# Optimization experiments

Hardware: AMD Instinct MI355X
Metric: run time of the kernel (lower is better)

The kernel has to match this reference:

```python
import jax, jax.numpy as jnp
import numpy as np
import math

N_NODES = 16384
N_EDGES = 200000
RADIUS = 2.5
BOX = 42.5
NUM_NEIGHBORS = 3.8

# irreps as (mul, l, parity); parity=-1 => irreps_sh = 1x0e+1x1o+1x2e+1x3o
IRREPS_SH = [(1,0,1),(1,1,-1),(1,2,1),(1,3,-1)]
GATE_IN = [(16,0,1),(16,0,-1),(8,0,1),(8,0,-1),(8,0,1),(8,0,-1),(16,1,-1),(16,1,1)]
GATE_OUT = [(16,0,1),(16,0,-1),(16,1,-1),(16,1,1)]
FINAL_OUT = [(1,1,-1)]

def _cg_coef(j1,m1,j2,m2,j3,m3):
    f = math.factorial
    pref = math.sqrt((2*j3+1)*f(j3+j1-j2)*f(j3-j1+j2)*f(j1+j2-j3)/f(j1+j2+j3+1))
    pref *= math.sqrt(f(j3+m3)*f(j3-m3)*f(j1-m1)*f(j1+m1)*f(j2-m2)*f(j2+m2))
    s = 0.0
    for k in range(j1+j2-j3+1):
        args = (k, j1+j2-j3-k, j1-m1-k, j2+m2-k, j3-j2+m1+k, j3-j1-m2+k)
        if min(args) < 0:
            continue
        d = 1
        for a in args:
            d *= f(a)
        s += (-1)**k / d
    return pref*s

def _cg_complex(l1,l2,l3):
    C = np.zeros((2*l1+1,2*l2+1,2*l3+1))
    for m1 in range(-l1,l1+1):
        for m2 in range(-l2,l2+1):
            m3 = m1+m2
            if abs(m3) <= l3:
                C[m1+l1,m2+l2,m3+l3] = _cg_coef(l1,m1,l2,m2,l3,m3)
    return C

def _u(l):
    # complex -> real spherical-harmonics change of basis (m ordered -l..l)
    U = np.zeros((2*l+1,2*l+1), dtype=complex)
    U[l,l] = 1.0
    for m in range(1,l+1):
        U[l+m,l+m] = (-1)**m/math.sqrt(2); U[l+m,l-m] = 1/math.sqrt(2)
        U[l-m,l-m] = 1j/math.sqrt(2);      U[l-m,l+m] = -1j*(-1)**m/math.sqrt(2)
    return U

_CG = {}
def cg_real(l1,l2,l3):
    k = (l1,l2,l3)
    if k not in _CG:
        C = np.einsum('au,bv,cw,uvw->abc', _u(l1), _u(l2), _u(l3).conj(), _cg_complex(l1,l2,l3).astype(complex))
        Cr = C.imag if np.abs(C.imag).sum() > np.abs(C.real).sum() else C.real
        _CG[k] = jnp.asarray(Cr.astype(np.float32))
    return _CG[k]

def _slices(irr):
    out, off = [], 0
    for (m,l,p) in irr:
        out.append((off,m,l,p)); off += m*(2*l+1)
    return out

def weight_numel(irr1, irr2, irro):
    n = 0
    for (_,m1,l1,p1) in _slices(irr1):
        for (_,m2,l2,p2) in _slices(irr2):
            for (_,mo,lo,po) in _slices(irro):
                if po == p1*p2 and abs(l1-l2) <= lo <= l1+l2:
                    n += m1*m2*mo
    return n

def fctp(x1, x2, w, irr1, irr2, irro):
    # fully-connected tensor product with per-edge external weights
    s1, s2, so = _slices(irr1), _slices(irr2), _slices(irro)
    E = x1.shape[0]
    chunks = [jnp.zeros((E,m,2*l+1), dtype=x1.dtype) for (_,m,l,_) in so]
    fan = [0]*len(so)
    woff = 0
    for (o1,m1,l1,p1) in s1:
        for (o2,m2,l2,p2) in s2:
            for io,(oo,mo,lo,po) in enumerate(so):
                if po == p1*p2 and abs(l1-l2) <= lo <= l1+l2:
                    nw = m1*m2*mo
                    wp = w[:, woff:woff+nw].reshape(E,m1,m2,mo); woff += nw
                    a = x1[:, o1:o1+m1*(2*l1+1)].reshape(E,m1,2*l1+1)
                    b = x2[:, o2:o2+m2*(2*l2+1)].reshape(E,m2,2*l2+1)
                    chunks[io] = chunks[io] + jnp.einsum('euvw,eui,evj,ijk->ewk', wp, a, b, cg_real(l1,l2,lo))
                    fan[io] += m1*m2
    return jnp.concatenate([(c/math.sqrt(f) if f > 0 else c).reshape(E,-1) for c,f in zip(chunks,fan)], axis=1)

def sph_harm(u):
    # real SH l=0..3, component normalization, m=-l..l, on unit vectors
    x, y, z = u[:,0], u[:,1], u[:,2]
    s3, s5, s15 = math.sqrt(3.), math.sqrt(5.), math.sqrt(15.)
    c33, c32, c31, c30, c3p2 = math.sqrt(35/8), math.sqrt(105.), math.sqrt(21/8), 0.5*math.sqrt(7.), 0.5*math.sqrt(105.)
    comps = [jnp.ones_like(x),
             s3*y, s3*z, s3*x,
             s15*x*y, s15*y*z, 0.5*s5*(3*z*z-1.), s15*x*z, 0.5*s15*(x*x-y*y),
             c33*y*(3*x*x-y*y), c32*x*y*z, c31*y*(5*z*z-1.), c30*(5*z**3-3*z),
             c31*x*(5*z*z-1.), c3p2*z*(x*x-y*y), c33*x*(x*x-3*y*y)]
    return jnp.stack(comps, axis=1)

def soft_one_hot(r):
    # basis='smooth_finite', cutoff=True, start=0.5, end=2.5, number=3
    centers = jnp.array([1.0, 1.5, 2.0], dtype=r.dtype)
    d = (r[:,None] - centers) / 0.5
    d2 = d*d
    inside = d2 < 1.0
    safe = jnp.where(inside, d2, 0.0)
    return jnp.where(inside, 1.14136*(math.e**2)*jnp.exp(1.0/(safe-1.0)), 0.0)

def gate_fn(x):
    se = jax.nn.relu(x[:,0:16]); so = jnp.abs(x[:,16:32])
    g = jnp.concatenate([jax.nn.relu(x[:,32:40]), jnp.tanh(x[:,40:48]),
                         jax.nn.relu(x[:,48:56]), jnp.tanh(x[:,56:64])], axis=1)  # [N,32]
    v1o = x[:,64:112].reshape(-1,16,3) * g[:,0:16,None]
    v1e = x[:,112:160].reshape(-1,16,3) * g[:,16:32,None]
    return jnp.concatenate([se, so, v1o.reshape(-1,48), v1e.reshape(-1,48)], axis=1)

def _forward(position, edge_src, edge_dst, W1, W2, W1f, W2f):
    evec = position[edge_src] - position[edge_dst]           # [E,3]
    r = jnp.linalg.norm(evec, axis=1)
    ea = sph_harm(evec / r[:,None])                          # [E,16]
    es = soft_one_hot(r) * math.sqrt(3.0)                    # [E,3]
    inv = 1.0/math.sqrt(NUM_NEIGHBORS)
    x = jax.ops.segment_sum(ea, edge_dst, num_segments=N_NODES) * inv      # [N,16]
    w = (jax.nn.relu(es @ W1 / math.sqrt(3.0)) @ W2) / math.sqrt(256.0)    # [E,272]
    e = fctp(x[edge_src], ea, w, IRREPS_SH, IRREPS_SH, GATE_IN)            # [E,160]
    x = jax.ops.segment_sum(e, edge_dst, num_segments=N_NODES) * inv       # [N,160]
    x = gate_fn(x)                                                          # [N,128]
    wf = (jax.nn.relu(es @ W1f / math.sqrt(3.0)) @ W2f) / math.sqrt(256.0) # [E,64]
    e = fctp(x[edge_src], ea, wf, GATE_OUT, IRREPS_SH, FINAL_OUT)          # [E,3]
    return jax.ops.segment_sum(e, edge_dst, num_segments=N_NODES) * inv    # [N,3]

def setup_inputs():
    rng = np.random.RandomState(0)
    pos = (rng.rand(N_NODES,3) * BOX).astype(np.float32)
    n2 = (pos**2).sum(1)
    src_l, dst_l = [], []
    for i0 in range(0, N_NODES, 2048):
        p = pos[i0:i0+2048]
        d2 = n2[i0:i0+2048,None] + n2[None,:] - 2.0*(p @ pos.T)
        ii, jj = np.nonzero(d2 < RADIUS*RADIUS)
        ii = ii + i0
        m = ii != jj
        src_l.append(jj[m]); dst_l.append(ii[m])
    src = np.concatenate(src_l); dst = np.concatenate(dst_l)
    if len(src) < N_EDGES:
        reps = int(np.ceil(N_EDGES/max(len(src),1)))
        src = np.tile(src, reps); dst = np.tile(dst, reps)
    src = src[:N_EDGES].astype(np.int32); dst = dst[:N_EDGES].astype(np.int32)
    key = jax.random.key(0)
    k1, k2, k3, k4 = jax.random.split(key, 4)
    w2n = weight_numel(IRREPS_SH, IRREPS_SH, GATE_IN)    # 272
    w2fn = weight_numel(GATE_OUT, IRREPS_SH, FINAL_OUT)  # 64
    return {"position": jnp.asarray(pos), "edge_src": jnp.asarray(src), "edge_dst": jnp.asarray(dst),
            "W1": jax.random.normal(k1,(3,256),jnp.float32), "W2": jax.random.normal(k2,(256,w2n),jnp.float32),
            "W1f": jax.random.normal(k3,(3,256),jnp.float32), "W2f": jax.random.normal(k4,(256,w2fn),jnp.float32)}

def reference(position, edge_src, edge_dst, W1, W2, W1f, W2f):
    return _forward(position, edge_src, edge_dst, W1, W2, W1f, W2f)
```

## Files before the change

### kernel.cpp

```cpp
#include <hip/hip_runtime.h>
#include <cmath>

#define T_TAB 3072
#define NN 16384
#define NG 4
#define CH2 16

struct CD { double re, im; };
constexpr CD cmul(CD a, CD b){ return {a.re*b.re - a.im*b.im, a.re*b.im + a.im*b.re}; }
constexpr CD cadd(CD a, CD b){ return {a.re+b.re, a.im+b.im}; }
constexpr CD conj_(CD a){ return {a.re, -a.im}; }
constexpr CD cscale(CD a, double s){ return {a.re*s, a.im*s}; }
constexpr double cfabs_(double x){ return x<0.0 ? -x : x; }
constexpr double csqrt_(double x){
  double g = x > 1.0 ? x : 1.0;
  for (int i=0;i<80;++i) g = 0.5*(g + x/g);
  return g;
}
constexpr double factd(int n){ double r=1.0; for(int i=2;i<=n;++i) r*=(double)i; return r; }

constexpr double cg_coef(int j1,int m1,int j2,int m2,int j3,int m3){
  double pref = csqrt_((2.0*j3+1.0)*factd(j3+j1-j2)*factd(j3-j1+j2)*factd(j1+j2-j3)/factd(j1+j2+j3+1));
  pref *= csqrt_(factd(j3+m3)*factd(j3-m3)*factd(j1-m1)*factd(j1+m1)*factd(j2-m2)*factd(j2+m2));
  double s=0.0;
  for(int k=0;k<=j1+j2-j3;++k){
    int a0=k,a1=j1+j2-j3-k,a2=j1-m1-k,a3=j2+m2-k,a4=j3-j2+m1+k,a5=j3-j1-m2+k;
    if(a0<0||a1<0||a2<0||a3<0||a4<0||a5<0) continue;
    double d=factd(a0)*factd(a1)*factd(a2)*factd(a3)*factd(a4)*factd(a5);
    s += ((k&1)?-1.0:1.0)/d;
  }
  return pref*s;
}

struct UMat { CD u[7][7]; };
constexpr UMat u_fill(int l){
  UMat M{};
  const double is2 = csqrt_(0.5);
  M.u[l][l] = CD{1.0, 0.0};
  for(int m=1;m<=l;++m){
    double sgn = (m&1)?-1.0:1.0;
    M.u[l+m][l+m] = CD{sgn*is2, 0.0};
    M.u[l+m][l-m] = CD{is2, 0.0};
    M.u[l-m][l-m] = CD{0.0, is2};
    M.u[l-m][l+m] = CD{0.0, -sgn*is2};
  }
  return M;
}

template<int L1,int L2,int L3>
struct FT { float v[(2*L1+1)*(2*L2+1)*(2*L3+1)]; };

template<int L1,int L2,int L3>
constexpr FT<L1,L2,L3> cg_real_ct(){
  constexpr int n1=2*L1+1, n2=2*L2+1, n3=2*L3+1;
  double Cc[7][7][7] = {};
  for(int m1=-L1;m1<=L1;++m1)
    for(int m2=-L2;m2<=L2;++m2){
      int m3=m1+m2;
      if(m3>=-L3&&m3<=L3) Cc[m1+L1][m2+L2][m3+L3]=cg_coef(L1,m1,L2,m2,L3,m3);
    }
  UMat U1 = u_fill(L1), U2 = u_fill(L2), U3 = u_fill(L3);
  CD Cr[7][7][7] = {};
  double sre=0.0, sim=0.0;
  for(int a=0;a<n1;++a)for(int b=0;b<n2;++b)for(int c=0;c<n3;++c){
    CD acc{0.0,0.0};
    for(int u=0;u<n1;++u)for(int v=0;v<n2;++v){
      int w = (u-L1)+(v-L2)+L3;
      if (w < 0 || w >= n3) continue;
      double cc = Cc[u][v][w];
      if (cc == 0.0) continue;
      acc = cadd(acc, cscale(cmul(cmul(U1.u[a][u],U2.u[b][v]),conj_(U3.u[c][w])), cc));
    }
    Cr[a][b][c] = acc;
    sre += cfabs_(acc.re); sim += cfabs_(acc.im);
  }
  FT<L1,L2,L3> out{};
  bool useim = sim > sre;
  for(int a=0;a<n1;++a)for(int b=0;b<n2;++b)for(int c=0;c<n3;++c)
    out.v[(a*n2+b)*n3+c] = (float)(useim ? Cr[a][b][c].im : Cr[a][b][c].re);
  return out;
}

constexpr auto CG000 = cg_real_ct<0,0,0>();
constexpr auto CG110 = cg_real_ct<1,1,0>();
constexpr auto CG220 = cg_real_ct<2,2,0>();
constexpr auto CG330 = cg_real_ct<3,3,0>();
constexpr auto CG011 = cg_real_ct<0,1,1>();
constexpr auto CG101 = cg_real_ct<1,0,1>();
constexpr auto CG111 = cg_real_ct<1,1,1>();
constexpr auto CG121 = cg_real_ct<1,2,1>();
constexpr auto CG211 = cg_real_ct<2,1,1>();
constexpr auto CG221 = cg_real_ct<2,2,1>();
constexpr auto CG231 = cg_real_ct<2,3,1>();
constexpr auto CG321 = cg_real_ct<3,2,1>();
constexpr auto CG331 = cg_real_ct<3,3,1>();

#define TERM(TBL, IDX, PROD, ACC) { float c_ = TBL.v[IDX]; if (c_ != 0.0f) ACC = fmaf((PROD), c_, ACC); }

__device__ __forceinline__ void afadd(float* p, float v){ unsafeAtomicAdd(p, v); }

__device__ __forceinline__ float soh(float r, float c){
  float d = (r - c) * 2.0f;
  float d2 = d*d;
  return (d2 < 1.0f) ? 1.14136f * expf(2.0f + 1.0f/(d2-1.0f)) : 0.0f;
}

__device__ __forceinline__ float bf_lo(unsigned u){ return __uint_as_float(u << 16); }
__device__ __forceinline__ float bf_hi(unsigned u){ return __uint_as_float(u & 0xFFFF0000u); }
__device__ __forceinline__ unsigned short bfpack(float v){
  unsigned b = __float_as_uint(v);
  return (unsigned short)((b + 0x7FFFu + ((b >> 16) & 1u)) >> 16);
}
__device__ __forceinline__ void unp8(uint4 u, float* o){
  o[0]=bf_lo(u.x); o[1]=bf_hi(u.x); o[2]=bf_lo(u.y); o[3]=bf_hi(u.y);
  o[4]=bf_lo(u.z); o[5]=bf_hi(u.z); o[6]=bf_lo(u.w); o[7]=bf_hi(u.w);
}

__device__ __forceinline__ void lane_sched(int lane, int q, int& col, int& slot){
  col = -1; slot = 31;
  if (lane < 16){
    int s = q >> 2, qq = q & 3;
    int a = 2*lane + s;
    const int base0[4] = {0, 64, 144, 224};
    col = base0[qq] + a; slot = qq;
  } else if (lane < 40){
    int idx = lane-16, u = idx/3, k = idx-3*u;
    const int wb[6] = {32,48,112,128,192,208};
    const int sb[6] = {4,7,10,13,16,19};
    if (q < 6){ col = wb[q]+u; slot = sb[q]+k; }
  } else if (lane < 52){
    int m = lane-40;
    int c0 = (q < 4) ? 2*m : 2*m+1;
    int u = c0/3, k = c0-3*u;
    int qq = (q < 4) ? q : q-4;
    if (qq < 3){
      const int wb[3] = {96,176,256};
      const int sb[3] = {22,25,28};
      col = wb[qq]+u; slot = sb[qq]+k;
    }
  }
}

#define TBLK 1008
#define RPB  65
__global__ __launch_bounds__(256) void k_stageA(
    const float* __restrict__ W1, const float* __restrict__ W2,
    const float* __restrict__ W1f, const float* __restrict__ W2f,
    float* __restrict__ tab1, unsigned short* __restrict__ tab2b,
    const int* __restrict__ dst, int E, int* __restrict__ rowptr,
    float* __restrict__ out, int outN)
{
  const int bid = blockIdx.x;
  if (bid < TBLK){
    const int jq  = bid / 12;
    const int t   = (bid % 12)*256 + threadIdx.x;
    const int j0  = jq*4;
    const float dr = 2.5f / (float)(T_TAB-1);
    const float r = (float)t * dr;
    const float e0 = soh(r,1.0f), e1 = soh(r,1.5f), e2 = soh(r,2.0f);
    float ax=0.f, ay=0.f, az=0.f, aw=0.f;
    if (j0 < 272){
      for (int cc=0; cc<256; ++cc){
        float h = fmaxf(fmaf(e0,W1[cc], fmaf(e1,W1[256+cc], e2*W1[512+cc])), 0.0f);
        float4 w = *(const float4*)(W2 + cc*272 + j0);
        ax = fmaf(h,w.x,ax); ay = fmaf(h,w.y,ay);
        az = fmaf(h,w.z,az); aw = fmaf(h,w.w,aw);
      }
      *(float4*)(tab1 + (size_t)t*272 + j0) = make_float4(ax*0.0625f, ay*0.0625f, az*0.0625f, aw*0.0625f);
    } else {
      const int jj = j0 - 272;
      for (int cc=0; cc<256; ++cc){
        float h = fmaxf(fmaf(e0,W1f[cc], fmaf(e1,W1f[256+cc], e2*W1f[512+cc])), 0.0f);
        float4 w = *(const float4*)(W2f + cc*64 + jj);
        ax = fmaf(h,w.x,ax); ay = fmaf(h,w.y,ay);
        az = fmaf(h,w.z,az); aw = fmaf(h,w.w,aw);
      }
      ushort4 o;
      o.x = bfpack(ax*0.0625f); o.y = bfpack(ay*0.0625f);
      o.z = bfpack(az*0.0625f); o.w = bfpack(aw*0.0625f);
      *(ushort4*)(tab2b + (size_t)t*64 + jj) = o;
    }
  } else if (bid < TBLK + RPB){
    const int n = (bid-TBLK)*256 + threadIdx.x;
    if (n > NN) return;
    int lo=0, hi=E;
    while (lo < hi){ int mid=(lo+hi)>>1; if (dst[mid] < n) lo=mid+1; else hi=mid; }
    rowptr[n]=lo;
  } else {
    const int idx = (bid - TBLK - RPB)*256 + threadIdx.x;
    if (idx < outN) out[idx] = 0.0f;
  }
}

#define PERB 6144
__global__ __launch_bounds__(256) void k_stageB(
    const float* __restrict__ tab1, unsigned short* __restrict__ tabP,
    const float* __restrict__ pos, const int* __restrict__ src,
    const int* __restrict__ rowptr, float* __restrict__ xacc)
{
  const int bid = blockIdx.x;
  if (bid < PERB){
    const int gid = bid*256 + threadIdx.x;
    const int t = gid >> 9, p = gid & 511;
    int col, slot;
    lane_sched(p>>3, p&7, col, slot);
    float v = (col >= 0) ? tab1[(size_t)t*272 + col] : 0.0f;
    tabP[gid] = bfpack(v);
    return;
  }
  const int tt = (bid-PERB)*256 + threadIdx.x;
  const int n = tt>>2, q = tt&3;
  if (n>=NN) return;
  const int r0=rowptr[n], r1=rowptr[n+1];
  const float pdx=pos[3*n], pdy=pos[3*n+1], pdz=pos[3*n+2];
  const float s3=1.73205081f, s5=2.23606798f, s15=3.87298335f;
  const float c33=2.09165007f, c32=10.2469508f, c31=1.62018517f, c30=1.32287566f, cp2=5.12347538f;
  float a0=0,a1=0,a2=0,a3=0,a4=0,a5=0,a6=0,a7=0,a8=0,a9=0,a10=0,a11=0,a12=0,a13=0,a14=0,a15=0;
  for (int e=r0+q; e<r1; e+=4){
    const int s=src[e];
    float ax=pos[3*s]-pdx, ay=pos[3*s+1]-pdy, az=pos[3*s+2]-pdz;
    float ir = 1.0f/sqrtf(ax*ax+ay*ay+az*az);
    float x=ax*ir, y=ay*ir, z=az*ir;
    a0+=1.0f; a1+=s3*y; a2+=s3*z; a3+=s3*x;
    a4+=s15*x*y; a5+=s15*y*z; a6+=0.5f*s5*(3.0f*z*z-1.0f); a7+=s15*x*z;
    a8+=0.5f*s15*(x*x-y*y); a9+=c33*y*(3.0f*x*x-y*y); a10+=c32*x*y*z; a11+=c31*y*(5.0f*z*z-1.0f);
    a12+=c30*(5.0f*z*z*z-3.0f*z); a13+=c31*x*(5.0f*z*z-1.0f); a14+=cp2*z*(x*x-y*y);
    a15+=c33*x*(x*x-3.0f*y*y);
  }
#define RED(v) v += __shfl_xor(v,1); v += __shfl_xor(v,2);
  RED(a0) RED(a1) RED(a2) RED(a3) RED(a4) RED(a5) RED(a6) RED(a7)
  RED(a8) RED(a9) RED(a10) RED(a11) RED(a12) RED(a13) RED(a14) RED(a15)
#undef RED
  float o0,o1,o2,o3;
  if (q==0){ o0=a0; o1=a1; o2=a2; o3=a3; }
  else if (q==1){ o0=a4; o1=a5; o2=a6; o3=a7; }
  else if (q==2){ o0=a8; o1=a9; o2=a10; o3=a11; }
  else { o0=a12; o1=a13; o2=a14; o3=a15; }
  *(float4*)(xacc + (size_t)n*16 + q*4) = make_float4(o0,o1,o2,o3);
}

__global__ __launch_bounds__(64) void k_tp1(
    const float* __restrict__ pos, const int* __restrict__ src,
    const int* __restrict__ rowptr, const float* __restrict__ xacc,
    const unsigned short* __restrict__ tabP, unsigned short* __restrict__ xgb)
{
  const int lane = threadIdx.x;
  const int nb   = blockIdx.x*NG;
  const int g    = lane >> 4, je = lane & 15;
  __shared__ float SI[NG][CH2][33];
  __shared__ int   SiT[NG][CH2];
  __shared__ float SG[NG][32];

  int rp[NG+1];
#pragma unroll
  for (int q=0;q<=NG;++q) rp[q] = rowptr[nb+q];
  int deg[NG];
#pragma unroll
  for (int q=0;q<NG;++q) deg[q] = rp[q+1]-rp[q];
  const int dmax = max(max(deg[0],deg[1]), max(deg[2],deg[3]));
  const int nch = (dmax + CH2 - 1) / CH2;

  int ioS[8];
#pragma unroll
  for (int p=0;p<8;++p){ int c_, s_; lane_sched(lane, p, c_, s_); ioS[p] = s_; }
  int gu0=16, gu1=16;
  if (lane >= 16 && lane < 40){ gu0 = 16 + (lane-16)/3; }
  else if (lane >= 40 && lane < 52){
    int m=lane-40; gu0 = 24 + (2*m)/3; gu1 = 24 + (2*m+1)/3;
  }

  const int mynode = nb + g;
  const float pdx=pos[3*mynode], pdy=pos[3*mynode+1], pdz=pos[3*mynode+2];
  float acc0[NG]={0,0,0,0}, acc1[NG]={0,0,0,0};

  for (int t=0; t<nch; ++t){
    __syncthreads();
    const int cg_ = deg[g] - t*CH2;
    if (je < cg_){
      const int e = rp[g] + t*CH2 + je;
      const int s = src[e];
      float ax=pos[3*s]-pdx, ay=pos[3*s+1]-pdy, az=pos[3*s+2]-pdz;
      float r = sqrtf(ax*ax+ay*ay+az*az);
      float ir = 1.0f/r;
      float x=ax*ir, y=ay*ir, z=az*ir;
      float f = r * 1228.4f;
      int i0 = (int)(f + 0.5f);
      if (i0 > T_TAB-1) i0 = T_TAB-1;

      const float s3=1.73205081f, s5=2.23606798f, s15=3.87298335f;
      const float c33=2.09165007f, c32=10.2469508f, c31=1.62018517f, c30=1.32287566f, cp2=5.12347538f;
      float Y[16];
      Y[0]=1.0f;
      Y[1]=s3*y; Y[2]=s3*z; Y[3]=s3*x;
      Y[4]=s15*x*y; Y[5]=s15*y*z; Y[6]=0.5f*s5*(3.0f*z*z-1.0f); Y[7]=s15*x*z; Y[8]=0.5f*s15*(x*x-y*y);
      Y[9]=c33*y*(3.0f*x*x-y*y); Y[10]=c32*x*y*z; Y[11]=c31*y*(5.0f*z*z-1.0f);
      Y[12]=c30*(5.0f*z*z*z-3.0f*z); Y[13]=c31*x*(5.0f*z*z-1.0f); Y[14]=cp2*z*(x*x-y*y);
      Y[15]=c33*x*(x*x-3.0f*y*y);
      float X[16];
      {
        const float inv = 0.5129891760f;
        const float4* q4 = (const float4*)(xacc + (size_t)s*16);
        float4 a=q4[0],b=q4[1],cc4=q4[2],d4=q4[3];
        X[0]=a.x*inv;X[1]=a.y*inv;X[2]=a.z*inv;X[3]=a.w*inv;
        X[4]=b.x*inv;X[5]=b.y*inv;X[6]=b.z*inv;X[7]=b.w*inv;
        X[8]=cc4.x*inv;X[9]=cc4.y*inv;X[10]=cc4.z*inv;X[11]=cc4.w*inv;
        X[12]=d4.x*inv;X[13]=d4.y*inv;X[14]=d4.z*inv;X[15]=d4.w*inv;
      }
      float* SS = SI[g][je];

      {
        float t0v = CG000.v[0]*X[0]*Y[0];
        float t1v=0.f, t2v=0.f, t3v=0.f;
#pragma unroll
        for (int i=0;i<3;++i)
#pragma unroll
          for (int j=0;j<3;++j) TERM(CG110, i*3+j, X[1+i]*Y[1+j], t1v)
#pragma unroll
        for (int i=0;i<5;++i)
#pragma unroll
          for (int j=0;j<5;++j) TERM(CG220, i*5+j, X[4+i]*Y[4+j], t2v)
#pragma unroll
        for (int i=0;i<7;++i)
#pragma unroll
          for (int j=0;j<7;++j) TERM(CG330, i*7+j, X[9+i]*Y[9+j], t3v)
        SS[0]=t0v; SS[1]=t1v; SS[2]=t2v; SS[3]=t3v;
      }
      {
        float v01[3]={0,0,0}, v10[3]={0,0,0}, v11[3]={0,0,0}, v12[3]={0,0,0},
              v21[3]={0,0,0}, v22[3]={0,0,0}, v23[3]={0,0,0}, v32[3]={0,0,0}, v33[3]={0,0,0};
#pragma unroll
        for (int j=0;j<3;++j){ float tt=X[0]*Y[1+j];
#pragma unroll
          for (int k=0;k<3;++k) TERM(CG011, j*3+k, tt, v01[k]) }
#pragma unroll
        for (int i=0;i<3;++i){ float tt=X[1+i]*Y[0];
#pragma unroll
          for (int k=0;k<3;++k) TERM(CG101, i*3+k, tt, v10[k]) }
#pragma unroll
        for (int i=0;i<3;++i)
#pragma unroll
          for (int j=0;j<3;++j){ float tt=X[1+i]*Y[1+j];
#pragma unroll
            for (int k=0;k<3;++k) TERM(CG111, (i*3+j)*3+k, tt, v11[k]) }
#pragma unroll
        for (int i=0;i<3;++i)
#pragma unroll
          for (int j=0;j<5;++j){ float tt=X[1+i]*Y[4+j];
#pragma unroll
            for (int k=0;k<3;++k) TERM(CG121, (i*5+j)*3+k, tt, v12[k]) }
#pragma unroll
        for (int i=0;i<5;++i)
#pragma unroll
          for (int j=0;j<3;++j){ float tt=X[4+i]*Y[1+j];
#pragma unroll
            for (int k=0;k<3;++k) TERM(CG211, (i*3+j)*3+k, tt, v21[k]) }
#pragma unroll
        for (int i=0;i<5;++i)
#pragma unroll
          for (int j=0;j<5;++j){ float tt=X[4+i]*Y[4+j];
#pragma unroll
            for (int k=0;k<3;++k) TERM(CG221, (i*5+j)*3+k, tt, v22[k]) }
#pragma unroll
        for (int i=0;i<5;++i)
#pragma unroll
          for (int j=0;j<7;++j){ float tt=X[4+i]*Y[9+j];
#pragma unroll
            for (int k=0;k<3;++k) TERM(CG231, (i*7+j)*3+k, tt, v23[k]) }
#pragma unroll
        for (int i=0;i<7;++i)
#pragma unroll
          for (int j=0;j<5;++j){ float tt=X[9+i]*Y[4+j];
#pragma unroll
            for (int k=0;k<3;++k) TERM(CG321, (i*5+j)*3+k, tt, v32[k]) }
#pragma unroll
        for (int i=0;i<7;++i)
#pragma unroll
          for (int j=0;j<7;++j){ float tt=X[9+i]*Y[9+j];
#pragma unroll
            for (int k=0;k<3;++k) TERM(CG331, (i*7+j)*3+k, tt, v33[k]) }
#pragma unroll
        for (int k=0;k<3;++k){
          SS[4+k]=v01[k]; SS[7+k]=v10[k]; SS[10+k]=v12[k]; SS[13+k]=v21[k];
          SS[16+k]=v23[k]; SS[19+k]=v32[k]; SS[22+k]=v11[k]; SS[25+k]=v22[k]; SS[28+k]=v33[k];
        }
      }
      SS[31]=0.0f;
      SiT[g][je]=i0;
    }
    __syncthreads();
#pragma unroll
    for (int q=0;q<NG;++q){
      const int cq = deg[q] - t*CH2;
#pragma unroll 4
      for (int j=0; j<CH2; ++j){
        if (j < cq){
          const float* __restrict__ I = SI[q][j];
          const unsigned short* __restrict__ wp = tabP + ((size_t)SiT[q][j]*512) + 8*lane;
          uint4 ra = *(const uint4*)wp;
          float a8[8];
          unp8(ra, a8);
          acc0[q] = fmaf(a8[0], I[ioS[0]], acc0[q]);
          acc0[q] = fmaf(a8[1], I[ioS[1]], acc0[q]);
          acc0[q] = fmaf(a8[2], I[ioS[2]], acc0[q]);
          acc0[q] = fmaf(a8[3], I[ioS[3]], acc0[q]);
          acc1[q] = fmaf(a8[4], I[ioS[4]], acc1[q]);
          acc1[q] = fmaf(a8[5], I[ioS[5]], acc1[q]);
          acc1[q] = fmaf(a8[6], I[ioS[6]], acc1[q]);
          acc1[q] = fmaf(a8[7], I[ioS[7]], acc1[q]);
        }
      }
    }
  }

  const float inv = 0.5129891760f;
  if (lane < 16){
#pragma unroll
    for (int q=0;q<NG;++q){
      SG[q][2*lane]   = acc0[q]*0.5f*inv;
      SG[q][2*lane+1] = acc1[q]*0.5f*inv;
    }
  }
  __syncthreads();
#pragma unroll
  for (int q=0;q<NG;++q){
    unsigned short* __restrict__ o = xgb + (size_t)(nb+q)*64;
    if (lane < 16){
      o[lane] = bfpack(fmaxf(SG[q][lane], 0.0f));
    } else if (lane < 40){
      int idx = lane-16;
      float vv = (acc0[q]+acc1[q])*0.4082482905f*inv;
      o[16+idx] = bfpack(vv * fmaxf(SG[q][gu0], 0.0f));
    } else if (lane < 52){
      int m = lane-40;
      float vv0 = acc0[q]*0.5773502692f*inv;
      float vv1 = acc1[q]*0.5773502692f*inv;
      o[40+2*m]   = bfpack(vv0 * fmaxf(SG[q][gu0], 0.0f));
      o[40+2*m+1] = bfpack(vv1 * fmaxf(SG[q][gu1], 0.0f));
    }
  }
}

__global__ __launch_bounds__(256) void k_tp2(
    const float* __restrict__ pos, const int* __restrict__ src, const int* __restrict__ dst, int E,
    const unsigned short* __restrict__ xgb, const unsigned short* __restrict__ tab2b,
    float* __restrict__ out)
{
  const int tid = threadIdx.x;
  const int e = blockIdx.x*256 + tid;
  __shared__ float S0[256], S1[256], S2[256];
  __shared__ int   D[256];
  float e2[3]={0,0,0};
  int dd = -1;
  if (e < E){
    const int s = src[e];
    dd = dst[e];
    float ax=pos[3*s]-pos[3*dd], ay=pos[3*s+1]-pos[3*dd+1], az=pos[3*s+2]-pos[3*dd+2];
    float r = sqrtf(ax*ax+ay*ay+az*az);
    float ir = 1.0f/r;
    float x=ax*ir, y=ay*ir, z=az*ir;
    float f = r * 1228.4f;
    int i0 = (int)(f + 0.5f);
    if (i0 > T_TAB-1) i0 = T_TAB-1;
    const unsigned short* __restrict__ w0 = tab2b + (size_t)i0*64;
    float wse[16], wA[8], wB[8], wC[8];
    unp8(*(const uint4*)(w0+0),  wse);
    unp8(*(const uint4*)(w0+8),  wse+8);
    unp8(*(const uint4*)(w0+16), wA);
    unp8(*(const uint4*)(w0+32), wB);
    unp8(*(const uint4*)(w0+48), wC);
    const float s3=1.73205081f, s5=2.23606798f, s15=3.87298335f;
    float Y[9];
    Y[0]=1.0f;
    Y[1]=s3*y; Y[2]=s3*z; Y[3]=s3*x;
    Y[4]=s15*x*y; Y[5]=s15*y*z; Y[6]=0.5f*s5*(3.0f*z*z-1.0f); Y[7]=s15*x*z; Y[8]=0.5f*s15*(x*x-y*y);
    const unsigned short* __restrict__ g = xgb + (size_t)s*64;
    float se[16], vo[24], ve[24];
    unp8(*(const uint4*)(g+0),  se);  unp8(*(const uint4*)(g+8),  se+8);
    unp8(*(const uint4*)(g+16), vo);  unp8(*(const uint4*)(g+24), vo+8); unp8(*(const uint4*)(g+32), vo+16);
    unp8(*(const uint4*)(g+40), ve);  unp8(*(const uint4*)(g+48), ve+8); unp8(*(const uint4*)(g+56), ve+16);

    float SA=0.0f;
#pragma unroll
    for (int u=0;u<16;++u) SA = fmaf(wse[u], se[u], SA);
    float AB[3]={0,0,0}, AC[3]={0,0,0}, AD[3]={0,0,0};
#pragma unroll
    for (int u=0;u<8;++u)
#pragma unroll
      for (int i=0;i<3;++i){
        AB[i]=fmaf(wA[u], vo[u*3+i], AB[i]);
        AC[i]=fmaf(wB[u], vo[u*3+i], AC[i]);
        AD[i]=fmaf(wC[u], ve[u*3+i], AD[i]);
      }
#pragma unroll
    for (int j=0;j<3;++j){ float t=SA*Y[1+j];
#pragma unroll
      for (int k=0;k<3;++k) TERM(CG011, j*3+k, t, e2[k]) }
#pragma unroll
    for (int i=0;i<3;++i){ float t=AB[i]*Y[0];
#pragma unroll
      for (int k=0;k<3;++k) TERM(CG101, i*3+k, t, e2[k]) }
#pragma unroll
    for (int i=0;i<3;++i)
#pragma unroll
      for (int j=0;j<5;++j){ float t=AC[i]*Y[4+j];
#pragma unroll
        for (int k=0;k<3;++k) TERM(CG121, (i*5+j)*3+k, t, e2[k]) }
#pragma unroll
    for (int i=0;i<3;++i)
#pragma unroll
      for (int j=0;j<3;++j){ float t=AD[i]*Y[1+j];
#pragma unroll
        for (int k=0;k<3;++k) TERM(CG111, (i*3+j)*3+k, t, e2[k]) }
  }
  S0[tid]=e2[0]; S1[tid]=e2[1]; S2[tid]=e2[2]; D[tid]=dd;
  __syncthreads();
  if (e < E && (tid==0 || D[tid-1] != dd)){
    float a0=0.f, a1=0.f, a2=0.f;
    int j = tid;
    while (j < 256 && D[j] == dd){ a0+=S0[j]; a1+=S1[j]; a2+=S2[j]; ++j; }
    const float sc = 0.0641236437f;
    afadd(out + (size_t)dd*3 + 0, a0*sc);
    afadd(out + (size_t)dd*3 + 1, a1*sc);
    afadd(out + (size_t)dd*3 + 2, a2*sc);
  }
}

extern "C" void kernel_launch(void* const* d_in, const int* in_sizes, int n_in,
                              void* d_out, int out_size, void* d_ws, size_t ws_size,
                              hipStream_t stream)
{
  (void)n_in; (void)ws_size;
  const float* pos = (const float*)d_in[0];
  const int*   src = (const int*)d_in[1];
  const int*   dst = (const int*)d_in[2];
  const float* W1  = (const float*)d_in[3];
  const float* W2  = (const float*)d_in[4];
  const float* W1f = (const float*)d_in[5];
  const float* W2f = (const float*)d_in[6];
  const int E = in_sizes[1];

  char* ws = (char*)d_ws;
  float* xacc  = (float*)ws;
  unsigned short* xgb = (unsigned short*)(xacc + (size_t)NN*16);
  float* tab1  = (float*)(xgb + (size_t)NN*64);
  unsigned short* tab2b = (unsigned short*)(tab1 + (size_t)T_TAB*272);
  unsigned short* tabP  = tab2b + (size_t)T_TAB*64;
  int*   rowptr= (int*)(tabP + (size_t)T_TAB*512);

  const int ozb = (out_size + 255) / 256;
  k_stageA<<<TBLK + RPB + ozb, 256, 0, stream>>>(W1, W2, W1f, W2f, tab1, tab2b,
                                                 dst, E, rowptr, (float*)d_out, out_size);
  k_stageB<<<PERB + (NN*4)/256, 256, 0, stream>>>(tab1, tabP, pos, src, rowptr, xacc);
  k_tp1<<<NN/NG, 64, 0, stream>>>(pos, src, rowptr, xacc, tabP, xgb);
  k_tp2<<<(E + 255) / 256, 256, 0, stream>>>(pos, src, dst, E, xgb, tab2b, (float*)d_out);
}
```

Measured before the change: 83.98 us.

## Fuse stage B into stage A and write packed bf16 table directly

The weight-table blocks now pack bf16 values straight into the per-lane scheduled table. They use a compile-time inverse map of the lane schedule, so the intermediate fp32 table and the repack pass go away. The rowptr binary search and the spherical-harmonic node accumulation move into the same launch: each 4-lane group finds its own row bounds and shares them by shuffle. This drops one kernel launch and a full fp32 table write and read. The risk is that packed-table slots with no source column are no longer written with zero, so stale workspace data may be read there.

```diff
diff --git a/kernel.cpp b/kernel.cpp
--- a/kernel.cpp
+++ b/kernel.cpp
@@ -97,26 +97,7 @@
 
 #define TERM(TBL, IDX, PROD, ACC) { float c_ = TBL.v[IDX]; if (c_ != 0.0f) ACC = fmaf((PROD), c_, ACC); }
 
-__device__ __forceinline__ void afadd(float* p, float v){ unsafeAtomicAdd(p, v); }
-
-__device__ __forceinline__ float soh(float r, float c){
-  float d = (r - c) * 2.0f;
-  float d2 = d*d;
-  return (d2 < 1.0f) ? 1.14136f * expf(2.0f + 1.0f/(d2-1.0f)) : 0.0f;
-}
-
-__device__ __forceinline__ float bf_lo(unsigned u){ return __uint_as_float(u << 16); }
-__device__ __forceinline__ float bf_hi(unsigned u){ return __uint_as_float(u & 0xFFFF0000u); }
-__device__ __forceinline__ unsigned short bfpack(float v){
-  unsigned b = __float_as_uint(v);
-  return (unsigned short)((b + 0x7FFFu + ((b >> 16) & 1u)) >> 16);
-}
-__device__ __forceinline__ void unp8(uint4 u, float* o){
-  o[0]=bf_lo(u.x); o[1]=bf_hi(u.x); o[2]=bf_lo(u.y); o[3]=bf_hi(u.y);
-  o[4]=bf_lo(u.z); o[5]=bf_hi(u.z); o[6]=bf_lo(u.w); o[7]=bf_hi(u.w);
-}
-
-__device__ __forceinline__ void lane_sched(int lane, int q, int& col, int& slot){
+__host__ __device__ constexpr void lane_sched(int lane, int q, int& col, int& slot){
   col = -1; slot = 31;
   if (lane < 16){
     int s = q >> 2, qq = q & 3;
@@ -141,14 +122,47 @@
   }
 }
 
+struct InvMap { short cnt[272]; short pos[272][3]; };
+constexpr InvMap build_inv(){
+  InvMap v{};
+  for (int c=0;c<272;++c) v.cnt[c]=0;
+  for (int p=0;p<512;++p){
+    int col=-1, slot=31;
+    lane_sched(p>>3, p&7, col, slot);
+    if (col>=0){ v.pos[col][v.cnt[col]] = (short)p; v.cnt[col] = (short)(v.cnt[col]+1); }
+  }
+  return v;
+}
+constexpr auto INV = build_inv();
+
+__device__ __forceinline__ void afadd(float* p, float v){ unsafeAtomicAdd(p, v); }
+
+__device__ __forceinline__ float soh(float r, float c){
+  float d = (r - c) * 2.0f;
+  float d2 = d*d;
+  return (d2 < 1.0f) ? 1.14136f * expf(2.0f + 1.0f/(d2-1.0f)) : 0.0f;
+}
+
+__device__ __forceinline__ float bf_lo(unsigned u){ return __uint_as_float(u << 16); }
+__device__ __forceinline__ float bf_hi(unsigned u){ return __uint_as_float(u & 0xFFFF0000u); }
+__device__ __forceinline__ unsigned short bfpack(float v){
+  unsigned b = __float_as_uint(v);
+  return (unsigned short)((b + 0x7FFFu + ((b >> 16) & 1u)) >> 16);
+}
+__device__ __forceinline__ void unp8(uint4 u, float* o){
+  o[0]=bf_lo(u.x); o[1]=bf_hi(u.x); o[2]=bf_lo(u.y); o[3]=bf_hi(u.y);
+  o[4]=bf_lo(u.z); o[5]=bf_hi(u.z); o[6]=bf_lo(u.w); o[7]=bf_hi(u.w);
+}
+
 #define TBLK 1008
-#define RPB  65
+#define XB   256
 __global__ __launch_bounds__(256) void k_stageA(
     const float* __restrict__ W1, const float* __restrict__ W2,
     const float* __restrict__ W1f, const float* __restrict__ W2f,
-    float* __restrict__ tab1, unsigned short* __restrict__ tab2b,
+    unsigned short* __restrict__ tabP, unsigned short* __restrict__ tab2b,
+    const float* __restrict__ pos, const int* __restrict__ src,
     const int* __restrict__ dst, int E, int* __restrict__ rowptr,
-    float* __restrict__ out, int outN)
+    float* __restrict__ xacc, float* __restrict__ out, int outN)
 {
   const int bid = blockIdx.x;
   if (bid < TBLK){
@@ -166,7 +180,15 @@
         ax = fmaf(h,w.x,ax); ay = fmaf(h,w.y,ay);
         az = fmaf(h,w.z,az); aw = fmaf(h,w.w,aw);
       }
-      *(float4*)(tab1 + (size_t)t*272 + j0) = make_float4(ax*0.0625f, ay*0.0625f, az*0.0625f, aw*0.0625f);
+      float val[4] = {ax*0.0625f, ay*0.0625f, az*0.0625f, aw*0.0625f};
+      unsigned short* __restrict__ rowp = tabP + (size_t)t*512;
+#pragma unroll
+      for (int k2=0;k2<4;++k2){
+        const int c = j0 + k2;
+        const unsigned short bv = bfpack(val[k2]);
+        const int cn = INV.cnt[c];
+        for (int i=0;i<cn;++i) rowp[INV.pos[c][i]] = bv;
+      }
     } else {
       const int jj = j0 - 272;
       for (int cc=0; cc<256; ++cc){
@@ -180,63 +202,47 @@
       o.z = bfpack(az*0.0625f); o.w = bfpack(aw*0.0625f);
       *(ushort4*)(tab2b + (size_t)t*64 + jj) = o;
     }
-  } else if (bid < TBLK + RPB){
-    const int n = (bid-TBLK)*256 + threadIdx.x;
-    if (n > NN) return;
+  } else if (bid < TBLK + XB){
+    const int tt = (bid-TBLK)*256 + threadIdx.x;
+    const int n = tt>>2, q = tt&3;
+    const int tgt = n + (q&1);
     int lo=0, hi=E;
-    while (lo < hi){ int mid=(lo+hi)>>1; if (dst[mid] < n) lo=mid+1; else hi=mid; }
-    rowptr[n]=lo;
+    while (lo<hi){ int mid=(lo+hi)>>1; if (dst[mid] < tgt) lo=mid+1; else hi=mid; }
+    if (q==0) rowptr[n] = lo;
+    if (q==1 && n==NN-1) rowptr[NN] = lo;
+    const int l = threadIdx.x & 63;
+    const int base = l & ~3;
+    const int r0 = __shfl(lo, base);
+    const int r1 = __shfl(lo, base+1);
+    const float pdx=pos[3*n], pdy=pos[3*n+1], pdz=pos[3*n+2];
+    const float s3=1.73205081f, s5=2.23606798f, s15=3.87298335f;
+    const float c33=2.09165007f, c32=10.2469508f, c31=1.62018517f, c30=1.32287566f, cp2=5.12347538f;
+    float a0=0,a1=0,a2=0,a3=0,a4=0,a5=0,a6=0,a7=0,a8=0,a9=0,a10=0,a11=0,a12=0,a13=0,a14=0,a15=0;
+    for (int e=r0+q; e<r1; e+=4){
+      const int s=src[e];
+      float ax=pos[3*s]-pdx, ay=pos[3*s+1]-pdy, az=pos[3*s+2]-pdz;
+      float ir = 1.0f/sqrtf(ax*ax+ay*ay+az*az);
+      float x=ax*ir, y=ay*ir, z=az*ir;
+      a0+=1.0f; a1+=s3*y; a2+=s3*z; a3+=s3*x;
+      a4+=s15*x*y; a5+=s15*y*z; a6+=0.5f*s5*(3.0f*z*z-1.0f); a7+=s15*x*z;
+      a8+=0.5f*s15*(x*x-y*y); a9+=c33*y*(3.0f*x*x-y*y); a10+=c32*x*y*z; a11+=c31*y*(5.0f*z*z-1.0f);
+      a12+=c30*(5.0f*z*z*z-3.0f*z); a13+=c31*x*(5.0f*z*z-1.0f); a14+=cp2*z*(x*x-y*y);
+      a15+=c33*x*(x*x-3.0f*y*y);
+    }
+#define RED(v) v += __shfl_xor(v,1); v += __shfl_xor(v,2);
+    RED(a0) RED(a1) RED(a2) RED(a3) RED(a4) RED(a5) RED(a6) RED(a7)
+    RED(a8) RED(a9) RED(a10) RED(a11) RED(a12) RED(a13) RED(a14) RED(a15)
+#undef RED
+    float o0,o1,o2,o3;
+    if (q==0){ o0=a0; o1=a1; o2=a2; o3=a3; }
+    else if (q==1){ o0=a4; o1=a5; o2=a6; o3=a7; }
+    else if (q==2){ o0=a8; o1=a9; o2=a10; o3=a11; }
+    else { o0=a12; o1=a13; o2=a14; o3=a15; }
+    *(float4*)(xacc + (size_t)n*16 + q*4) = make_float4(o0,o1,o2,o3);
   } else {
-    const int idx = (bid - TBLK - RPB)*256 + threadIdx.x;
+    const int idx = (bid - TBLK - XB)*256 + threadIdx.x;
     if (idx < outN) out[idx] = 0.0f;
   }
-}
-
-#define PERB 6144
-__global__ __launch_bounds__(256) void k_stageB(
-    const float* __restrict__ tab1, unsigned short* __restrict__ tabP,
-    const float* __restrict__ pos, const int* __restrict__ src,
-    const int* __restrict__ rowptr, float* __restrict__ xacc)
-{
-  const int bid = blockIdx.x;
-  if (bid < PERB){
-    const int gid = bid*256 + threadIdx.x;
-    const int t = gid >> 9, p = gid & 511;
-    int col, slot;
-    lane_sched(p>>3, p&7, col, slot);
-    float v = (col >= 0) ? tab1[(size_t)t*272 + col] : 0.0f;
-    tabP[gid] = bfpack(v);
-    return;
-  }
-  const int tt = (bid-PERB)*256 + threadIdx.x;
-  const int n = tt>>2, q = tt&3;
-  if (n>=NN) return;
-  const int r0=rowptr[n], r1=rowptr[n+1];
-  const float pdx=pos[3*n], pdy=pos[3*n+1], pdz=pos[3*n+2];
-  const float s3=1.73205081f, s5=2.23606798f, s15=3.87298335f;
-  const float c33=2.09165007f, c32=10.2469508f, c31=1.62018517f, c30=1.32287566f, cp2=5.12347538f;
-  float a0=0,a1=0,a2=0,a3=0,a4=0,a5=0,a6=0,a7=0,a8=0,a9=0,a10=0,a11=0,a12=0,a13=0,a14=0,a15=0;
-  for (int e=r0+q; e<r1; e+=4){
-    const int s=src[e];
-    float ax=pos[3*s]-pdx, ay=pos[3*s+1]-pdy, az=pos[3*s+2]-pdz;
-    float ir = 1.0f/sqrtf(ax*ax+ay*ay+az*az);
-    float x=ax*ir, y=ay*ir, z=az*ir;
-    a0+=1.0f; a1+=s3*y; a2+=s3*z; a3+=s3*x;
-    a4+=s15*x*y; a5+=s15*y*z; a6+=0.5f*s5*(3.0f*z*z-1.0f); a7+=s15*x*z;
-    a8+=0.5f*s15*(x*x-y*y); a9+=c33*y*(3.0f*x*x-y*y); a10+=c32*x*y*z; a11+=c31*y*(5.0f*z*z-1.0f);
-    a12+=c30*(5.0f*z*z*z-3.0f*z); a13+=c31*x*(5.0f*z*z-1.0f); a14+=cp2*z*(x*x-y*y);
-    a15+=c33*x*(x*x-3.0f*y*y);
-  }
-#define RED(v) v += __shfl_xor(v,1); v += __shfl_xor(v,2);
-  RED(a0) RED(a1) RED(a2) RED(a3) RED(a4) RED(a5) RED(a6) RED(a7)
-  RED(a8) RED(a9) RED(a10) RED(a11) RED(a12) RED(a13) RED(a14) RED(a15)
-#undef RED
-  float o0,o1,o2,o3;
-  if (q==0){ o0=a0; o1=a1; o2=a2; o3=a3; }
-  else if (q==1){ o0=a4; o1=a5; o2=a6; o3=a7; }
-  else if (q==2){ o0=a8; o1=a9; o2=a10; o3=a11; }
-  else { o0=a12; o1=a13; o2=a14; o3=a15; }
-  *(float4*)(xacc + (size_t)n*16 + q*4) = make_float4(o0,o1,o2,o3);
 }
 
 __global__ __launch_bounds__(64) void k_tp1(
@@ -262,7 +268,7 @@
 
   int ioS[8];
 #pragma unroll
-  for (int p=0;p<8;++p){ int c_, s_; lane_sched(lane, p, c_, s_); ioS[p] = s_; }
+  for (int p=0;p<8;++p){ int c_=-1, s_=31; lane_sched(lane, p, c_, s_); ioS[p] = s_; }
   int gu0=16, gu1=16;
   if (lane >= 16 && lane < 40){ gu0 = 16 + (lane-16)/3; }
   else if (lane >= 40 && lane < 52){
@@ -542,15 +548,14 @@
   char* ws = (char*)d_ws;
   float* xacc  = (float*)ws;
   unsigned short* xgb = (unsigned short*)(xacc + (size_t)NN*16);
-  float* tab1  = (float*)(xgb + (size_t)NN*64);
-  unsigned short* tab2b = (unsigned short*)(tab1 + (size_t)T_TAB*272);
+  unsigned short* tab2b = xgb + (size_t)NN*64;
   unsigned short* tabP  = tab2b + (size_t)T_TAB*64;
   int*   rowptr= (int*)(tabP + (size_t)T_TAB*512);
 
   const int ozb = (out_size + 255) / 256;
-  k_stageA<<<TBLK + RPB + ozb, 256, 0, stream>>>(W1, W2, W1f, W2f, tab1, tab2b,
-                                                 dst, E, rowptr, (float*)d_out, out_size);
-  k_stageB<<<PERB + (NN*4)/256, 256, 0, stream>>>(tab1, tabP, pos, src, rowptr, xacc);
+  k_stageA<<<TBLK + XB + ozb, 256, 0, stream>>>(W1, W2, W1f, W2f, tabP, tab2b,
+                                                pos, src, dst, E, rowptr, xacc,
+                                                (float*)d_out, out_size);
   k_tp1<<<NN/NG, 64, 0, stream>>>(pos, src, rowptr, xacc, tabP, xgb);
   k_tp2<<<(E + 255) / 256, 256, 0, stream>>>(pos, src, dst, E, xgb, tab2b, (float*)d_out);
 }
```

New measurement: 77.02 us. -8.3%, faster.
